# Kernel optimization log

Hardware: AMD Instinct MI355X
Metric: run time of the kernel (lower is better)

The kernel has to match this reference:

```python
import jax, jax.numpy as jnp
import numpy as np

B, S, D = 4, 1024, 1024
L, H, DK, DV, DFF = 2, 8, 128, 128, 2048
MASK_VALUE = -1e-30
LN_EPS = 1e-14  # K.epsilon()**2 with K.epsilon()=1e-7


def _glorot(key, shape):
    fan_in, fan_out = shape[-2], shape[-1]
    lim = np.sqrt(6.0 / (fan_in + fan_out)).astype(np.float32)
    return jax.random.uniform(key, shape, jnp.float32, -lim, lim)


def setup_inputs() -> dict:
    key = jax.random.key(0)
    ks = jax.random.split(key, 8)
    return {
        "x": jax.random.normal(ks[0], (B, S, D), jnp.float32),
        "mask": jnp.ones((B, S), jnp.float32),
        "Wq": _glorot(ks[1], (L, H, D, DK)),
        "Wk": _glorot(ks[2], (L, H, D, DK)),
        "Wv": _glorot(ks[3], (L, H, D, DV)),
        "Wo": _glorot(ks[4], (L, H * DV, D)),
        "W1": _glorot(ks[5], (L, D, DFF)),
        "b1": jnp.zeros((L, DFF), jnp.float32),
        "W2": _glorot(ks[6], (L, DFF, D)),
        "b2": jnp.zeros((L, D), jnp.float32),
        "gamma": jnp.ones((2 * L,), jnp.float32),
        "beta": jnp.zeros((2 * L,), jnp.float32),
    }


def _layernorm(x, g, b):
    mean = jnp.mean(x, axis=-1, keepdims=True)
    var = jnp.mean(jnp.square(x - mean), axis=-1, keepdims=True)
    return (x - mean) / jnp.sqrt(var + LN_EPS) * g + b


def reference(x, mask, Wq, Wk, Wv, Wo, W1, b1, W2, b2, gamma, beta):
    m = mask[:, None, None, :]  # [B,1,1,S] broadcast over heads and query positions
    num_layers = Wq.shape[0]
    for i in range(num_layers):
        # All heads at once (faithful to the per-head loop: identical math)
        q = jnp.einsum("bsd,hdk->bhsk", x, Wq[i])
        k = jnp.einsum("bsd,hdk->bhsk", x, Wk[i])
        v = jnp.einsum("bsd,hdv->bhsv", x, Wv[i])
        A = jnp.einsum("bhsk,bhtk->bhst", q, k)  # NOTE: no 1/sqrt(dk) scaling in original
        A = m * A + (1.0 - m) * MASK_VALUE
        A = jax.nn.softmax(A, axis=-1)
        o = jnp.einsum("bhst,bhtv->bhsv", A, v)
        conc = o.transpose(0, 2, 1, 3).reshape(x.shape[0], x.shape[1], -1)  # [B,S,H*DV]
        proj = conc @ Wo[i]
        x = _layernorm(x + proj, gamma[2 * i], beta[2 * i])
        ffn = jax.nn.relu(x @ W1[i] + b1[i]) @ W2[i] + b2[i]
        x = _layernorm(x + ffn, gamma[2 * i + 1], beta[2 * i + 1])
    return x
```

## Files before the change

kernel.cpp:

```cpp
#include <hip/hip_runtime.h>
#include <hip/hip_bf16.h>


typedef __bf16 bf16_t;
typedef bf16_t bf16x8 __attribute__((ext_vector_type(8)));
typedef bf16_t bf16x4v __attribute__((ext_vector_type(4)));
typedef float f32x4 __attribute__((ext_vector_type(4)));

#define MFMA16(a, b, c) __builtin_amdgcn_mfma_f32_16x16x32_bf16((a), (b), (c), 0, 0, 0)

__device__ __align__(256) unsigned char g_ws[(size_t)192 << 20];

#define MBOFF(x) ((size_t)(x) << 20)
#define OFF_X32 MBOFF(0)
#define OFF_XB_HI MBOFF(16)
#define OFF_XB_LO MBOFF(24)
#define OFF_QKV_HI MBOFF(32)
#define OFF_QKV_LO MBOFF(56)
#define OFF_VT_HI MBOFF(80)
#define OFF_VT_LO MBOFF(88)
#define OFF_CONC_HI MBOFF(96)
#define OFF_CONC_LO MBOFF(104)
#define OFF_TMP MBOFF(112)
#define OFF_H_HI MBOFF(128)
#define OFF_H_LO MBOFF(144)
#define OFF_WQKV_HI MBOFF(160)
#define OFF_WQKV_LO MBOFF(166)
#define OFF_WO_HI MBOFF(172)
#define OFF_WO_LO MBOFF(174)
#define OFF_W1_HI MBOFF(176)
#define OFF_W1_LO MBOFF(180)
#define OFF_W2_HI MBOFF(184)
#define OFF_W2_LO MBOFF(188)

__device__ __forceinline__ void split2(float v, bf16_t& h, bf16_t& l) {
  h = (bf16_t)v;
  l = (bf16_t)(v - (float)h);
}

__device__ __forceinline__ void gl2lds16(const bf16_t* g, bf16_t* l) {
  __builtin_amdgcn_global_load_lds(
      (const __attribute__((address_space(1))) unsigned int*)(g),
      (__attribute__((address_space(3))) unsigned int*)(l), 16, 0, 0);
}

template <int EPI>
__global__ __launch_bounds__(512) void gemm_bt(
    size_t a_hi, size_t a_lo, size_t b_hi, size_t b_lo,
    size_t c0o, size_t c1o, const float* __restrict__ bias, int M, int N, int K) {
  const bf16_t* Ah = (const bf16_t*)(g_ws + a_hi);
  const bf16_t* Al = (const bf16_t*)(g_ws + a_lo);
  const bf16_t* Bh = (const bf16_t*)(g_ws + b_hi);
  const bf16_t* Bl = (const bf16_t*)(g_ws + b_lo);
  float* Cf = (float*)(g_ws + c0o);
  bf16_t* Ch = (bf16_t*)(g_ws + c0o);
  bf16_t* Cl = (bf16_t*)(g_ws + c1o);
  __shared__ __align__(16) bf16_t Ash[128 * 32];
  __shared__ __align__(16) bf16_t Asl[128 * 32];
  __shared__ __align__(16) bf16_t Bsh[128 * 32];
  __shared__ __align__(16) bf16_t Bsl[128 * 32];
  const int tid = threadIdx.x;
  const int wave = tid >> 6, lane = tid & 63;
  const int quad = lane >> 4, l16 = lane & 15;
  const int wm = wave & 3, wn = wave >> 2;
  const int m0 = blockIdx.y * 128, n0 = blockIdx.x * 128;
  const int srow = wave * 16 + (lane >> 2);
  const int scp = (lane & 3) ^ ((srow >> 1) & 3);
  const long agoff = (long)(m0 + srow) * K + scp * 8;
  const long bgoff = (long)(n0 + srow) * K + scp * 8;
  bf16_t* ldsA = Ash + wave * 512;
  bf16_t* ldsAl = Asl + wave * 512;
  bf16_t* ldsB = Bsh + wave * 512;
  bf16_t* ldsBl = Bsl + wave * 512;
  int aOff[2], bOff[4];
#pragma unroll
  for (int mt = 0; mt < 2; ++mt) {
    int R = wm * 32 + mt * 16 + l16;
    aOff[mt] = R * 32 + ((quad ^ ((R >> 1) & 3)) * 8);
  }
#pragma unroll
  for (int nt = 0; nt < 4; ++nt) {
    int R = wn * 64 + nt * 16 + l16;
    bOff[nt] = R * 32 + ((quad ^ ((R >> 1) & 3)) * 8);
  }
  f32x4 acc[2][4] = {};

  for (int k0 = 0; k0 < K; k0 += 32) {
    gl2lds16(Ah + agoff + k0, ldsA);
    gl2lds16(Al + agoff + k0, ldsAl);
    gl2lds16(Bh + bgoff + k0, ldsB);
    gl2lds16(Bl + bgoff + k0, ldsBl);
    __syncthreads();
    bf16x8 ah[2], al[2], bhf[4], blf[4];
#pragma unroll
    for (int mt = 0; mt < 2; ++mt) {
      ah[mt] = *(const bf16x8*)(Ash + aOff[mt]);
      al[mt] = *(const bf16x8*)(Asl + aOff[mt]);
    }
#pragma unroll
    for (int nt = 0; nt < 4; ++nt) {
      bhf[nt] = *(const bf16x8*)(Bsh + bOff[nt]);
      blf[nt] = *(const bf16x8*)(Bsl + bOff[nt]);
    }
#pragma unroll
    for (int mt = 0; mt < 2; ++mt)
#pragma unroll
      for (int nt = 0; nt < 4; ++nt) {
        acc[mt][nt] = MFMA16(ah[mt], bhf[nt], acc[mt][nt]);
        acc[mt][nt] = MFMA16(ah[mt], blf[nt], acc[mt][nt]);
        acc[mt][nt] = MFMA16(al[mt], bhf[nt], acc[mt][nt]);
      }
    __syncthreads();
  }

#pragma unroll
  for (int mt = 0; mt < 2; ++mt) {
    const int row0 = m0 + wm * 32 + mt * 16 + quad * 4;
#pragma unroll
    for (int nt = 0; nt < 4; ++nt) {
      const int col = n0 + wn * 64 + nt * 16 + l16;
      float bv = (EPI >= 2) ? bias[col] : 0.0f;
#pragma unroll
      for (int r = 0; r < 4; ++r) {
        float v = acc[mt][nt][r] + bv;
        if (EPI == 2) v = fmaxf(v, 0.0f);
        long off = (long)(row0 + r) * N + col;
        if (EPI == 0 || EPI == 3) {
          Cf[off] = v;
        } else {
          bf16_t h, l;
          split2(v, h, l);
          Ch[off] = h;
          Cl[off] = l;
        }
      }
    }
  }
}

__global__ __launch_bounds__(256) void attn_kernel(const float* __restrict__ mask) {
  const bf16_t* QKVh = (const bf16_t*)(g_ws + OFF_QKV_HI);
  const bf16_t* QKVl = (const bf16_t*)(g_ws + OFF_QKV_LO);
  const bf16_t* VTh = (const bf16_t*)(g_ws + OFF_VT_HI);
  const bf16_t* VTl = (const bf16_t*)(g_ws + OFF_VT_LO);
  bf16_t* conch = (bf16_t*)(g_ws + OFF_CONC_HI);
  bf16_t* concl = (bf16_t*)(g_ws + OFF_CONC_LO);
  __shared__ __align__(16) bf16_t Ksh[64 * 128];
  __shared__ __align__(16) bf16_t Ksl[64 * 128];
  __shared__ __align__(16) bf16_t Vsh[128 * 64];
  __shared__ __align__(16) bf16_t Vsl[128 * 64];
  __shared__ __align__(16) bf16_t Ps[4][16 * 72];
  const int tid = threadIdx.x;
  const int wave = tid >> 6, lane = tid & 63;
  const int quad = lane >> 4, l16 = lane & 15;
  const int q0 = blockIdx.x * 64;
  const int bh = blockIdx.y, b = bh >> 3, h = bh & 7;

  bf16x8 qfh[4], qfl[4];
  const long qgbase = ((long)(b * 1024) + q0 + wave * 16 + l16) * 3072 + h * 128;
#pragma unroll
  for (int ks = 0; ks < 4; ++ks) {
    qfh[ks] = *(const bf16x8*)(QKVh + qgbase + ks * 32 + quad * 8);
    qfl[ks] = *(const bf16x8*)(QKVl + qgbase + ks * 32 + quad * 8);
  }

  const int sKrow4 = wave * 16 + (lane >> 4);
  const int sVrow = wave * 32 + (lane >> 3);
  const int sVc = (lane & 7) ^ (sVrow & 7);
  const long vgbase = (long)bh * 131072 + (long)sVrow * 1024 + sVc * 8;

  f32x4 o[8] = {};
  float mi[4] = {-1e30f, -1e30f, -1e30f, -1e30f};
  float li[4] = {0.f, 0.f, 0.f, 0.f};

  for (int t0 = 0; t0 < 1024; t0 += 64) {
#pragma unroll
    for (int j = 0; j < 4; ++j) {
      const int r = sKrow4 + j * 4;
      const int c = (lane & 15) ^ ((r & 7) * 2);
      const long kg = ((long)(b * 1024) + t0 + r) * 3072 + 1024 + h * 128 + c * 8;
      gl2lds16(QKVh + kg, Ksh + (wave * 16 + j * 4) * 128);
      gl2lds16(QKVl + kg, Ksl + (wave * 16 + j * 4) * 128);
    }
#pragma unroll
    for (int j = 0; j < 4; ++j) {
      const long vg = vgbase + (long)(j * 8) * 1024 + t0;
      gl2lds16(VTh + vg, Vsh + (wave * 32 + j * 8) * 64);
      gl2lds16(VTl + vg, Vsl + (wave * 32 + j * 8) * 64);
    }
    __syncthreads();
    f32x4 s4[4] = {};
#pragma unroll
    for (int nt = 0; nt < 4; ++nt) {
      const int krow = nt * 16 + l16;
      const int ksw = (krow & 7) * 2;
#pragma unroll
      for (int ks = 0; ks < 4; ++ks) {
        const int so = krow * 128 + (((ks * 4 + quad) ^ ksw) * 8);
        bf16x8 kfh = *(const bf16x8*)(Ksh + so);
        bf16x8 kfl = *(const bf16x8*)(Ksl + so);
        s4[nt] = MFMA16(qfh[ks], kfh, s4[nt]);
        s4[nt] = MFMA16(qfh[ks], kfl, s4[nt]);
        s4[nt] = MFMA16(qfl[ks], kfh, s4[nt]);
      }
    }
#pragma unroll
    for (int nt = 0; nt < 4; ++nt) {
      float mv = mask[b * 1024 + t0 + nt * 16 + l16];
      float addv = (1.0f - mv) * (-1e-30f);
#pragma unroll
      for (int r = 0; r < 4; ++r) s4[nt][r] = mv * s4[nt][r] + addv;
    }
#pragma unroll
    for (int r = 0; r < 4; ++r) {
      float mx = fmaxf(fmaxf(s4[0][r], s4[1][r]), fmaxf(s4[2][r], s4[3][r]));
#pragma unroll
      for (int off = 1; off < 16; off <<= 1) mx = fmaxf(mx, __shfl_xor(mx, off, 64));
      float mnew = fmaxf(mi[r], mx);
      float alpha = __expf(mi[r] - mnew);
      float rs = 0.0f;
#pragma unroll
      for (int nt = 0; nt < 4; ++nt) {
        float p = __expf(s4[nt][r] - mnew);
        s4[nt][r] = p;
        rs += p;
      }
#pragma unroll
      for (int off = 1; off < 16; off <<= 1) rs += __shfl_xor(rs, off, 64);
      li[r] = li[r] * alpha + rs;
      mi[r] = mnew;
#pragma unroll
      for (int on = 0; on < 8; ++on) o[on][r] *= alpha;
    }
#pragma unroll
    for (int nt = 0; nt < 4; ++nt)
#pragma unroll
      for (int r = 0; r < 4; ++r)
        Ps[wave][(quad * 4 + r) * 72 + nt * 16 + l16] = (bf16_t)s4[nt][r];
    bf16x8 pf[2];
#pragma unroll
    for (int k2 = 0; k2 < 2; ++k2)
      pf[k2] = *(const bf16x8*)(&Ps[wave][l16 * 72 + k2 * 32 + quad * 8]);
#pragma unroll
    for (int k2 = 0; k2 < 2; ++k2) {
#pragma unroll
      for (int on = 0; on < 8; ++on) {
        const int vrow = on * 16 + l16;
        const int so = vrow * 64 + (((k2 * 4 + quad) ^ (vrow & 7)) * 8);
        bf16x8 vfh = *(const bf16x8*)(Vsh + so);
        bf16x8 vfl = *(const bf16x8*)(Vsl + so);
        o[on] = MFMA16(pf[k2], vfh, o[on]);
        o[on] = MFMA16(pf[k2], vfl, o[on]);
      }
    }
    __syncthreads();
  }
  const int srow_o = q0 + wave * 16 + quad * 4;
#pragma unroll
  for (int r = 0; r < 4; ++r) {
    float inv = 1.0f / li[r];
#pragma unroll
    for (int on = 0; on < 8; ++on) {
      float v = o[on][r] * inv;
      bf16_t hh, ll;
      split2(v, hh, ll);
      long off = (long)(b * 1024 + srow_o + r) * 1024 + h * 128 + on * 16 + l16;
      conch[off] = hh;
      concl[off] = ll;
    }
  }
}

__global__ __launch_bounds__(256) void ln_kernel(
    const float* __restrict__ gamma, const float* __restrict__ beta, int gidx,
    float* __restrict__ extf) {
  const float* xres = (const float*)(g_ws + OFF_X32);
  const float* y = (const float*)(g_ws + OFF_TMP);
  float* xout = (float*)(g_ws + OFF_X32);
  bf16_t* xbh = (bf16_t*)(g_ws + OFF_XB_HI);
  bf16_t* xbl = (bf16_t*)(g_ws + OFF_XB_LO);
  const int row = blockIdx.x, tid = threadIdx.x;
  const int wave = tid >> 6, lane = tid & 63;
  const long base = (long)row * 1024 + tid * 4;
  float4 xv = *(const float4*)(xres + base);
  float4 yv = *(const float4*)(y + base);
  float v0 = xv.x + yv.x, v1 = xv.y + yv.y, v2 = xv.z + yv.z, v3 = xv.w + yv.w;
  float s1 = v0 + v1 + v2 + v3;
  float s2 = v0 * v0 + v1 * v1 + v2 * v2 + v3 * v3;
#pragma unroll
  for (int off = 1; off < 64; off <<= 1) {
    s1 += __shfl_xor(s1, off, 64);
    s2 += __shfl_xor(s2, off, 64);
  }
  __shared__ __align__(16) float r1[4], r2[4];
  if (lane == 0) { r1[wave] = s1; r2[wave] = s2; }
  __syncthreads();
  s1 = r1[0] + r1[1] + r1[2] + r1[3];
  s2 = r2[0] + r2[1] + r2[2] + r2[3];
  const float mean = s1 * (1.0f / 1024.0f);
  float var = s2 * (1.0f / 1024.0f) - mean * mean;
  var = fmaxf(var, 0.0f);
  const float inv = rsqrtf(var + 1e-14f);
  const float g = gamma[gidx], be = beta[gidx];
  float o0 = (v0 - mean) * inv * g + be;
  float o1 = (v1 - mean) * inv * g + be;
  float o2 = (v2 - mean) * inv * g + be;
  float o3 = (v3 - mean) * inv * g + be;
  float4 ov = {o0, o1, o2, o3};
  *(float4*)(xout + base) = ov;
  if (extf) {
    *(float4*)(extf + base) = ov;
  } else {
    bf16_t h0, l0, h1, l1, h2, l2, h3, l3;
    split2(o0, h0, l0); split2(o1, h1, l1);
    split2(o2, h2, l2); split2(o3, h3, l3);
    bf16x4v hv = {h0, h1, h2, h3};
    bf16x4v lv = {l0, l1, l2, l3};
    *(bf16x4v*)(xbh + base) = hv;
    *(bf16x4v*)(xbl + base) = lv;
  }
}

__global__ __launch_bounds__(256) void cast_f2b(const float* __restrict__ in) {
  float* out = (float*)(g_ws + OFF_X32);
  bf16_t* outh = (bf16_t*)(g_ws + OFF_XB_HI);
  bf16_t* outl = (bf16_t*)(g_ws + OFF_XB_LO);
  long i = ((long)blockIdx.x * 256 + threadIdx.x) * 4;
  float4 v = *(const float4*)(in + i);
  *(float4*)(out + i) = v;
  bf16_t h0, l0, h1, l1, h2, l2, h3, l3;
  split2(v.x, h0, l0); split2(v.y, h1, l1);
  split2(v.z, h2, l2); split2(v.w, h3, l3);
  bf16x4v hv = {h0, h1, h2, h3};
  bf16x4v lv = {l0, l1, l2, l3};
  *(bf16x4v*)(outh + i) = hv;
  *(bf16x4v*)(outl + i) = lv;
}

__global__ __launch_bounds__(256) void transp_split(
    const float* __restrict__ in, size_t oh_off, size_t ol_off, int R, int C) {
  bf16_t* oh = (bf16_t*)(g_ws + oh_off);
  bf16_t* ol = (bf16_t*)(g_ws + ol_off);
  __shared__ float tile[32][33];
  const int tx = threadIdx.x, ty = threadIdx.y;
  const int c0 = blockIdx.x * 32, r0 = blockIdx.y * 32;
#pragma unroll
  for (int j = 0; j < 4; ++j)
    tile[ty + j * 8][tx] = in[(long)(r0 + ty + j * 8) * C + c0 + tx];
  __syncthreads();
#pragma unroll
  for (int j = 0; j < 4; ++j) {
    float v = tile[tx][ty + j * 8];
    bf16_t h, l;
    split2(v, h, l);
    long off = (long)(c0 + ty + j * 8) * R + r0 + tx;
    oh[off] = h;
    ol[off] = l;
  }
}

__global__ __launch_bounds__(256) void qkvw_trans(
    const float* __restrict__ Wq, const float* __restrict__ Wk,
    const float* __restrict__ Wv) {
  bf16_t* oh = (bf16_t*)(g_ws + OFF_WQKV_HI);
  bf16_t* ol = (bf16_t*)(g_ws + OFF_WQKV_LO);
  __shared__ float tile[32][33];
  const int tx = threadIdx.x, ty = threadIdx.y;
  const int z = blockIdx.z, mat = z >> 3, h = z & 7;
  const float* src = (mat == 0 ? Wq : (mat == 1 ? Wk : Wv)) + h * 131072;
  const int c0 = blockIdx.x * 32, r0 = blockIdx.y * 32;
#pragma unroll
  for (int j = 0; j < 4; ++j)
    tile[ty + j * 8][tx] = src[(r0 + ty + j * 8) * 128 + c0 + tx];
  __syncthreads();
  const int nbase = mat * 1024 + h * 128;
#pragma unroll
  for (int j = 0; j < 4; ++j) {
    float v = tile[tx][ty + j * 8];
    bf16_t hh, ll;
    split2(v, hh, ll);
    long off = (long)(nbase + c0 + ty + j * 8) * 1024 + r0 + tx;
    oh[off] = hh;
    ol[off] = ll;
  }
}

__global__ __launch_bounds__(256) void vt_trans() {
  const bf16_t* QKVh = (const bf16_t*)(g_ws + OFF_QKV_HI);
  const bf16_t* QKVl = (const bf16_t*)(g_ws + OFF_QKV_LO);
  bf16_t* VTh = (bf16_t*)(g_ws + OFF_VT_HI);
  bf16_t* VTl = (bf16_t*)(g_ws + OFF_VT_LO);
  __shared__ bf16_t th[32][34];
  __shared__ bf16_t tl[32][34];
  const int tx = threadIdx.x, ty = threadIdx.y;
  const int bh = blockIdx.z, b = bh >> 3, h = bh & 7;
  const int s0 = blockIdx.x * 32, v0 = blockIdx.y * 32;
#pragma unroll
  for (int j = 0; j < 4; ++j) {
    long src = ((long)(b * 1024) + s0 + ty + j * 8) * 3072 + 2048 + h * 128 + v0 + tx;
    th[ty + j * 8][tx] = QKVh[src];
    tl[ty + j * 8][tx] = QKVl[src];
  }
  __syncthreads();
#pragma unroll
  for (int j = 0; j < 4; ++j) {
    long off = (long)bh * 131072 + (long)(v0 + ty + j * 8) * 1024 + s0 + tx;
    VTh[off] = th[tx][ty + j * 8];
    VTl[off] = tl[tx][ty + j * 8];
  }
}

extern "C" void kernel_launch(void* const* d_in, const int* in_sizes, int n_in,
                              void* d_out, int out_size, void* d_ws, size_t ws_size,
                              hipStream_t stream) {
  const float* x_in = (const float*)d_in[0];
  const float* mask = (const float*)d_in[1];
  const float* Wq = (const float*)d_in[2];
  const float* Wk = (const float*)d_in[3];
  const float* Wv = (const float*)d_in[4];
  const float* Wo = (const float*)d_in[5];
  const float* W1 = (const float*)d_in[6];
  const float* b1 = (const float*)d_in[7];
  const float* W2 = (const float*)d_in[8];
  const float* b2 = (const float*)d_in[9];
  const float* gamma = (const float*)d_in[10];
  const float* beta = (const float*)d_in[11];
  float* out = (float*)d_out;
  (void)d_ws; (void)ws_size; (void)in_sizes; (void)n_in; (void)out_size;

  const dim3 tb(32, 8);
  cast_f2b<<<4096, 256, 0, stream>>>(x_in);

  for (int l = 0; l < 2; ++l) {
    qkvw_trans<<<dim3(4, 32, 24), tb, 0, stream>>>(
        Wq + (long)l * 1048576, Wk + (long)l * 1048576, Wv + (long)l * 1048576);
    transp_split<<<dim3(32, 32), tb, 0, stream>>>(Wo + (long)l * 1048576,
                                                  OFF_WO_HI, OFF_WO_LO, 1024, 1024);
    transp_split<<<dim3(64, 32), tb, 0, stream>>>(W1 + (long)l * 2097152,
                                                  OFF_W1_HI, OFF_W1_LO, 1024, 2048);
    transp_split<<<dim3(32, 64), tb, 0, stream>>>(W2 + (long)l * 2097152,
                                                  OFF_W2_HI, OFF_W2_LO, 2048, 1024);

    gemm_bt<1><<<dim3(24, 32), 512, 0, stream>>>(
        OFF_XB_HI, OFF_XB_LO, OFF_WQKV_HI, OFF_WQKV_LO,
        OFF_QKV_HI, OFF_QKV_LO, nullptr, 4096, 3072, 1024);
    vt_trans<<<dim3(32, 4, 32), tb, 0, stream>>>();
    attn_kernel<<<dim3(16, 32), 256, 0, stream>>>(mask);
    gemm_bt<0><<<dim3(8, 32), 512, 0, stream>>>(
        OFF_CONC_HI, OFF_CONC_LO, OFF_WO_HI, OFF_WO_LO,
        OFF_TMP, 0, nullptr, 4096, 1024, 1024);
    ln_kernel<<<4096, 256, 0, stream>>>(gamma, beta, 2 * l, nullptr);
    gemm_bt<2><<<dim3(16, 32), 512, 0, stream>>>(
        OFF_XB_HI, OFF_XB_LO, OFF_W1_HI, OFF_W1_LO,
        OFF_H_HI, OFF_H_LO, b1 + l * 2048, 4096, 2048, 1024);
    gemm_bt<3><<<dim3(8, 32), 512, 0, stream>>>(
        OFF_H_HI, OFF_H_LO, OFF_W2_HI, OFF_W2_LO,
        OFF_TMP, 0, b2 + l * 1024, 4096, 1024, 2048);
    ln_kernel<<<4096, 256, 0, stream>>>(gamma, beta, 2 * l + 1,
                                        (l == 1) ? out : nullptr);
  }
}
```

Baseline: 879.6 us.

## Restructure GEMM to 4 waves with register A tiles; drop V low split

The GEMM now runs 256 threads with each wave computing a 64x64 tile. A fragments are loaded straight from global memory into registers instead of through LDS, and only B is staged in shared memory. MFMAs are grouped by hi/lo term. Separately, the attention path drops the low-order bf16 half of V, removing the VT_lo transpose, its loads and one MFMA per PV step. This reduces precision of the P·V product, and the direct global A loads are uncoalesced per wave, which may stress memory.

```diff
diff --git a/kernel.cpp b/kernel.cpp
--- a/kernel.cpp
+++ b/kernel.cpp
@@ -18,7 +18,6 @@
 #define OFF_QKV_HI MBOFF(32)
 #define OFF_QKV_LO MBOFF(56)
 #define OFF_VT_HI MBOFF(80)
-#define OFF_VT_LO MBOFF(88)
 #define OFF_CONC_HI MBOFF(96)
 #define OFF_CONC_LO MBOFF(104)
 #define OFF_TMP MBOFF(112)
@@ -45,7 +44,7 @@
 }
 
 template <int EPI>
-__global__ __launch_bounds__(512) void gemm_bt(
+__global__ __launch_bounds__(256) void gemm_bt(
     size_t a_hi, size_t a_lo, size_t b_hi, size_t b_lo,
     size_t c0o, size_t c1o, const float* __restrict__ bias, int M, int N, int K) {
   const bf16_t* Ah = (const bf16_t*)(g_ws + a_hi);
@@ -55,67 +54,70 @@
   float* Cf = (float*)(g_ws + c0o);
   bf16_t* Ch = (bf16_t*)(g_ws + c0o);
   bf16_t* Cl = (bf16_t*)(g_ws + c1o);
-  __shared__ __align__(16) bf16_t Ash[128 * 32];
-  __shared__ __align__(16) bf16_t Asl[128 * 32];
   __shared__ __align__(16) bf16_t Bsh[128 * 32];
   __shared__ __align__(16) bf16_t Bsl[128 * 32];
   const int tid = threadIdx.x;
   const int wave = tid >> 6, lane = tid & 63;
   const int quad = lane >> 4, l16 = lane & 15;
-  const int wm = wave & 3, wn = wave >> 2;
+  const int wm = wave & 1, wn = wave >> 1;
   const int m0 = blockIdx.y * 128, n0 = blockIdx.x * 128;
-  const int srow = wave * 16 + (lane >> 2);
-  const int scp = (lane & 3) ^ ((srow >> 1) & 3);
-  const long agoff = (long)(m0 + srow) * K + scp * 8;
-  const long bgoff = (long)(n0 + srow) * K + scp * 8;
-  bf16_t* ldsA = Ash + wave * 512;
-  bf16_t* ldsAl = Asl + wave * 512;
-  bf16_t* ldsB = Bsh + wave * 512;
-  bf16_t* ldsBl = Bsl + wave * 512;
-  int aOff[2], bOff[4];
-#pragma unroll
-  for (int mt = 0; mt < 2; ++mt) {
-    int R = wm * 32 + mt * 16 + l16;
-    aOff[mt] = R * 32 + ((quad ^ ((R >> 1) & 3)) * 8);
-  }
+
+  long arow[4];
+#pragma unroll
+  for (int mt = 0; mt < 4; ++mt)
+    arow[mt] = (long)(m0 + wm * 64 + mt * 16 + l16) * K + quad * 8;
+
+  int bOff[4];
 #pragma unroll
   for (int nt = 0; nt < 4; ++nt) {
     int R = wn * 64 + nt * 16 + l16;
     bOff[nt] = R * 32 + ((quad ^ ((R >> 1) & 3)) * 8);
   }
-  f32x4 acc[2][4] = {};
+  f32x4 acc[4][4] = {};
 
   for (int k0 = 0; k0 < K; k0 += 32) {
-    gl2lds16(Ah + agoff + k0, ldsA);
-    gl2lds16(Al + agoff + k0, ldsAl);
-    gl2lds16(Bh + bgoff + k0, ldsB);
-    gl2lds16(Bl + bgoff + k0, ldsBl);
+    bf16x8 ah[4], al4[4];
+#pragma unroll
+    for (int mt = 0; mt < 4; ++mt) {
+      ah[mt] = *(const bf16x8*)(Ah + arow[mt] + k0);
+      al4[mt] = *(const bf16x8*)(Al + arow[mt] + k0);
+    }
+#pragma unroll
+    for (int j = 0; j < 2; ++j) {
+      const int r = wave * 32 + j * 16 + (lane >> 2);
+      const int c = (lane & 3) ^ ((r >> 1) & 3);
+      const long bg = (long)(n0 + r) * K + k0 + c * 8;
+      gl2lds16(Bh + bg, Bsh + (wave * 32 + j * 16) * 32);
+      gl2lds16(Bl + bg, Bsl + (wave * 32 + j * 16) * 32);
+    }
     __syncthreads();
-    bf16x8 ah[2], al[2], bhf[4], blf[4];
-#pragma unroll
-    for (int mt = 0; mt < 2; ++mt) {
-      ah[mt] = *(const bf16x8*)(Ash + aOff[mt]);
-      al[mt] = *(const bf16x8*)(Asl + aOff[mt]);
-    }
+    bf16x8 bh4[4], bl4[4];
 #pragma unroll
     for (int nt = 0; nt < 4; ++nt) {
-      bhf[nt] = *(const bf16x8*)(Bsh + bOff[nt]);
-      blf[nt] = *(const bf16x8*)(Bsl + bOff[nt]);
-    }
-#pragma unroll
-    for (int mt = 0; mt < 2; ++mt)
-#pragma unroll
-      for (int nt = 0; nt < 4; ++nt) {
-        acc[mt][nt] = MFMA16(ah[mt], bhf[nt], acc[mt][nt]);
-        acc[mt][nt] = MFMA16(ah[mt], blf[nt], acc[mt][nt]);
-        acc[mt][nt] = MFMA16(al[mt], bhf[nt], acc[mt][nt]);
-      }
+      bh4[nt] = *(const bf16x8*)(Bsh + bOff[nt]);
+      bl4[nt] = *(const bf16x8*)(Bsl + bOff[nt]);
+    }
+#pragma unroll
+    for (int mt = 0; mt < 4; ++mt)
+#pragma unroll
+      for (int nt = 0; nt < 4; ++nt)
+        acc[mt][nt] = MFMA16(ah[mt], bh4[nt], acc[mt][nt]);
+#pragma unroll
+    for (int mt = 0; mt < 4; ++mt)
+#pragma unroll
+      for (int nt = 0; nt < 4; ++nt)
+        acc[mt][nt] = MFMA16(ah[mt], bl4[nt], acc[mt][nt]);
+#pragma unroll
+    for (int mt = 0; mt < 4; ++mt)
+#pragma unroll
+      for (int nt = 0; nt < 4; ++nt)
+        acc[mt][nt] = MFMA16(al4[mt], bh4[nt], acc[mt][nt]);
     __syncthreads();
   }
 
 #pragma unroll
-  for (int mt = 0; mt < 2; ++mt) {
-    const int row0 = m0 + wm * 32 + mt * 16 + quad * 4;
+  for (int mt = 0; mt < 4; ++mt) {
+    const int row0 = m0 + wm * 64 + mt * 16 + quad * 4;
 #pragma unroll
     for (int nt = 0; nt < 4; ++nt) {
       const int col = n0 + wn * 64 + nt * 16 + l16;
@@ -142,13 +144,11 @@
   const bf16_t* QKVh = (const bf16_t*)(g_ws + OFF_QKV_HI);
   const bf16_t* QKVl = (const bf16_t*)(g_ws + OFF_QKV_LO);
   const bf16_t* VTh = (const bf16_t*)(g_ws + OFF_VT_HI);
-  const bf16_t* VTl = (const bf16_t*)(g_ws + OFF_VT_LO);
   bf16_t* conch = (bf16_t*)(g_ws + OFF_CONC_HI);
   bf16_t* concl = (bf16_t*)(g_ws + OFF_CONC_LO);
   __shared__ __align__(16) bf16_t Ksh[64 * 128];
   __shared__ __align__(16) bf16_t Ksl[64 * 128];
   __shared__ __align__(16) bf16_t Vsh[128 * 64];
-  __shared__ __align__(16) bf16_t Vsl[128 * 64];
   __shared__ __align__(16) bf16_t Ps[4][16 * 72];
   const int tid = threadIdx.x;
   const int wave = tid >> 6, lane = tid & 63;
@@ -186,7 +186,6 @@
     for (int j = 0; j < 4; ++j) {
       const long vg = vgbase + (long)(j * 8) * 1024 + t0;
       gl2lds16(VTh + vg, Vsh + (wave * 32 + j * 8) * 64);
-      gl2lds16(VTl + vg, Vsl + (wave * 32 + j * 8) * 64);
     }
     __syncthreads();
     f32x4 s4[4] = {};
@@ -248,9 +247,7 @@
         const int vrow = on * 16 + l16;
         const int so = vrow * 64 + (((k2 * 4 + quad) ^ (vrow & 7)) * 8);
         bf16x8 vfh = *(const bf16x8*)(Vsh + so);
-        bf16x8 vfl = *(const bf16x8*)(Vsl + so);
         o[on] = MFMA16(pf[k2], vfh, o[on]);
-        o[on] = MFMA16(pf[k2], vfl, o[on]);
       }
     }
     __syncthreads();
@@ -387,11 +384,8 @@
 
 __global__ __launch_bounds__(256) void vt_trans() {
   const bf16_t* QKVh = (const bf16_t*)(g_ws + OFF_QKV_HI);
-  const bf16_t* QKVl = (const bf16_t*)(g_ws + OFF_QKV_LO);
   bf16_t* VTh = (bf16_t*)(g_ws + OFF_VT_HI);
-  bf16_t* VTl = (bf16_t*)(g_ws + OFF_VT_LO);
   __shared__ bf16_t th[32][34];
-  __shared__ bf16_t tl[32][34];
   const int tx = threadIdx.x, ty = threadIdx.y;
   const int bh = blockIdx.z, b = bh >> 3, h = bh & 7;
   const int s0 = blockIdx.x * 32, v0 = blockIdx.y * 32;
@@ -399,14 +393,12 @@
   for (int j = 0; j < 4; ++j) {
     long src = ((long)(b * 1024) + s0 + ty + j * 8) * 3072 + 2048 + h * 128 + v0 + tx;
     th[ty + j * 8][tx] = QKVh[src];
-    tl[ty + j * 8][tx] = QKVl[src];
   }
   __syncthreads();
 #pragma unroll
   for (int j = 0; j < 4; ++j) {
     long off = (long)bh * 131072 + (long)(v0 + ty + j * 8) * 1024 + s0 + tx;
     VTh[off] = th[tx][ty + j * 8];
-    VTl[off] = tl[tx][ty + j * 8];
   }
 }
 
@@ -441,19 +433,19 @@
     transp_split<<<dim3(32, 64), tb, 0, stream>>>(W2 + (long)l * 2097152,
                                                   OFF_W2_HI, OFF_W2_LO, 2048, 1024);
 
-    gemm_bt<1><<<dim3(24, 32), 512, 0, stream>>>(
+    gemm_bt<1><<<dim3(24, 32), 256, 0, stream>>>(
         OFF_XB_HI, OFF_XB_LO, OFF_WQKV_HI, OFF_WQKV_LO,
         OFF_QKV_HI, OFF_QKV_LO, nullptr, 4096, 3072, 1024);
     vt_trans<<<dim3(32, 4, 32), tb, 0, stream>>>();
     attn_kernel<<<dim3(16, 32), 256, 0, stream>>>(mask);
-    gemm_bt<0><<<dim3(8, 32), 512, 0, stream>>>(
+    gemm_bt<0><<<dim3(8, 32), 256, 0, stream>>>(
         OFF_CONC_HI, OFF_CONC_LO, OFF_WO_HI, OFF_WO_LO,
         OFF_TMP, 0, nullptr, 4096, 1024, 1024);
     ln_kernel<<<4096, 256, 0, stream>>>(gamma, beta, 2 * l, nullptr);
-    gemm_bt<2><<<dim3(16, 32), 512, 0, stream>>>(
+    gemm_bt<2><<<dim3(16, 32), 256, 0, stream>>>(
         OFF_XB_HI, OFF_XB_LO, OFF_W1_HI, OFF_W1_LO,
         OFF_H_HI, OFF_H_LO, b1 + l * 2048, 4096, 2048, 1024);
-    gemm_bt<3><<<dim3(8, 32), 512, 0, stream>>>(
+    gemm_bt<3><<<dim3(8, 32), 256, 0, stream>>>(
         OFF_H_HI, OFF_H_LO, OFF_W2_HI, OFF_W2_LO,
         OFF_TMP, 0, b2 + l * 1024, 4096, 1024, 2048);
     ln_kernel<<<4096, 256, 0, stream>>>(gamma, beta, 2 * l + 1,
```

After: 1.130 ms. 28.5% more time.
